# Optimization experiments

Measured on AMD Instinct MI355X. Metric: run time of the kernel, lower is better.

The kernel has to match this reference:

```python
import jax, jax.numpy as jnp
import numpy as np

# Static network layout: inputs occupy columns [0, I), hidden [I, N-O), outputs [N-O, N)
B = 16384  # batch size
N = 1024   # total neurons
I = 128    # input neurons
O = 64     # output neurons
REFRACTORY = 0.9


def _activate(x, act_ids):
    """Vectorized per-neuron heterogeneous activation.
    act_ids: 0=relu, 1=tanh, 2=sigmoid, 3=identity.
    Replaces the original serial per-neuron getattr dispatch loop."""
    r = jax.nn.relu(x)
    t = jnp.tanh(x)
    s = jax.nn.sigmoid(x)
    return jnp.select([act_ids == 0, act_ids == 1, act_ids == 2], [r, t, s], x)


def setup_inputs() -> dict:
    key = jax.random.key(0)
    k0, k1, k2, k3, k4 = jax.random.split(key, 5)
    return {
        "prev_states": jax.random.normal(k0, (B, N), jnp.float32),
        "input_values": jax.random.normal(k1, (B, I), jnp.float32),
        "weight_matrix": jax.random.normal(k2, (N, N), jnp.float32) * 0.05,
        "biases": jax.random.normal(k3, (N,), jnp.float32) * 0.1,
        "act_ids": jax.random.randint(k4, (N,), 0, 4, dtype=jnp.int32),
    }


def reference(prev_states, input_values, weight_matrix, biases, act_ids):
    # _apply_refractory_factor on hidden cols + _assign_input_values on input cols
    states = jnp.concatenate(
        [input_values,
         prev_states[:, I:N - O] * REFRACTORY,
         prev_states[:, N - O:]],
        axis=1)  # [B, N]
    # total_input = states @ W + b
    total = states @ weight_matrix + biases  # [B, N]
    # activation applied to every non-input neuron; input neurons keep their state
    activated = _activate(total, act_ids[None, :])  # [B, N]
    new_states = jnp.concatenate([states[:, :I], activated[:, I:]], axis=1)
    # return output-layer slice
    return new_states[:, N - O:]
```

## Files before the change

### kernel.cpp

```cpp
#include <hip/hip_runtime.h>
#include <math.h>

#define BATCH 16384
#define NN    1024
#define NI    128
#define NO    64
#define REFR  0.9f

typedef float  f32x4  __attribute__((ext_vector_type(4)));
typedef __bf16 bf16x8 __attribute__((ext_vector_type(8)));

__global__ __launch_bounds__(256) void pack_w_kernel(const float* __restrict__ W,
                                                     __bf16* __restrict__ wsB) {
    int idx = blockIdx.x * 256 + threadIdx.x;
    int k = idx >> 6;
    int n = idx & 63;
    float v = W[(size_t)k * NN + (NN - NO) + n];
    int kc = k >> 5;
    if (kc >= 4 && kc < 30) v *= REFR;
    int kk = k & 31;
    int r3 = kk >> 3;
    int j  = kk & 7;
    int tn = n >> 4;
    int l  = r3 * 16 + (n & 15);
    wsB[(size_t)(((kc * 4 + tn) * 64 + l) * 8 + j)] = (__bf16)v;
}

__device__ inline float activate(float x, int id) {
    if (id == 0) return fmaxf(x, 0.0f);
    if (id == 1) return tanhf(x);
    if (id == 2) return 1.0f / (1.0f + __expf(-x));
    return x;
}

__global__ __launch_bounds__(256, 4) void fused_rnn_kernel(
    const float* __restrict__ prev,
    const float* __restrict__ inp,
    const __bf16* __restrict__ wsB,
    const float* __restrict__ bias,
    const int*  __restrict__ act,
    float* __restrict__ out)
{
    const int lane = threadIdx.x & 63;
    const int wv   = threadIdx.x >> 6;
    const int m    = lane & 15;
    const int q    = lane >> 4;
    const int row0 = blockIdx.x * 16;
    const int rowA = row0 + m;

    const float* prow = prev + (size_t)rowA * NN;
    const float* irow = inp  + (size_t)rowA * NI;
    const bf16x8* Bf  = (const bf16x8*)wsB;

    f32x4 acc[4];
    acc[0] = (f32x4){0.f, 0.f, 0.f, 0.f};
    acc[1] = acc[0]; acc[2] = acc[0]; acc[3] = acc[0];

    const int qo = q * 8;

#pragma unroll
    for (int i = 0; i < 8; ++i) {
        const int kc = wv * 8 + i;
        const float* srcRow = (kc < 4) ? irow : prow;

        const float4* p = (const float4*)(srcRow + kc * 32 + qo);
        float4 f0 = p[0];
        float4 f1 = p[1];
        bf16x8 a;
        a[0] = (__bf16)f0.x; a[1] = (__bf16)f0.y;
        a[2] = (__bf16)f0.z; a[3] = (__bf16)f0.w;
        a[4] = (__bf16)f1.x; a[5] = (__bf16)f1.y;
        a[6] = (__bf16)f1.z; a[7] = (__bf16)f1.w;

        const bf16x8* bp = Bf + (size_t)kc * 256 + lane;
        acc[0] = __builtin_amdgcn_mfma_f32_16x16x32_bf16(a, bp[0],   acc[0], 0, 0, 0);
        acc[1] = __builtin_amdgcn_mfma_f32_16x16x32_bf16(a, bp[64],  acc[1], 0, 0, 0);
        acc[2] = __builtin_amdgcn_mfma_f32_16x16x32_bf16(a, bp[128], acc[2], 0, 0, 0);
        acc[3] = __builtin_amdgcn_mfma_f32_16x16x32_bf16(a, bp[192], acc[3], 0, 0, 0);
    }

    __shared__ float red[4][16][68];
#pragma unroll
    for (int t = 0; t < 4; ++t) {
#pragma unroll
        for (int r = 0; r < 4; ++r) {
            red[wv][q * 4 + r][t * 16 + m] = acc[t][r];
        }
    }
    __syncthreads();

    const int orow = threadIdx.x >> 4;
    const int oc   = (threadIdx.x & 15) * 4;

    f32x4 s;
    {
        const f32x4* p0 = (const f32x4*)&red[0][orow][oc];
        const f32x4* p1 = (const f32x4*)&red[1][orow][oc];
        const f32x4* p2 = (const f32x4*)&red[2][orow][oc];
        const f32x4* p3 = (const f32x4*)&red[3][orow][oc];
        s = *p0 + *p1 + *p2 + *p3;
    }

    const float* bo = bias + (NN - NO);
    const int*   ao = act  + (NN - NO);
    f32x4 o;
#pragma unroll
    for (int c = 0; c < 4; ++c) {
        o[c] = activate(s[c] + bo[oc + c], ao[oc + c]);
    }
    *(f32x4*)(out + (size_t)(row0 + orow) * NO + oc) = o;
}

extern "C" void kernel_launch(void* const* d_in, const int* in_sizes, int n_in,
                              void* d_out, int out_size, void* d_ws, size_t ws_size,
                              hipStream_t stream) {
    const float* prev = (const float*)d_in[0];
    const float* inp  = (const float*)d_in[1];
    const float* W    = (const float*)d_in[2];
    const float* bias = (const float*)d_in[3];
    const int*   act  = (const int*)  d_in[4];
    float* out = (float*)d_out;
    __bf16* wsB = (__bf16*)d_ws;

    pack_w_kernel<<<256, 256, 0, stream>>>(W, wsB);

    fused_rnn_kernel<<<BATCH / 16, 256, 0, stream>>>(prev, inp, wsB, bias, act, out);
}
```

Baseline: 114.3 us.

## Process 32 rows per block so each loaded weight fragment feeds two MFMAs

Each block now handles 32 batch rows instead of 16. Every wave computes two 16-row tiles, so each loaded B fragment is reused across two MFMAs, which halves weight-fragment load traffic per row. The grid shrinks to 512 blocks, launch bounds drop to 2 blocks per CU, and the shared reduction buffer doubles. The cost is more registers and fewer blocks, which can weaken latency hiding in a kernel that is mostly bound by the float32 activation reads.

```diff
diff --git a/kernel.cpp b/kernel.cpp
--- a/kernel.cpp
+++ b/kernel.cpp
@@ -33,7 +33,7 @@
     return x;
 }
 
-__global__ __launch_bounds__(256, 4) void fused_rnn_kernel(
+__global__ __launch_bounds__(256, 2) void fused_rnn_kernel(
     const float* __restrict__ prev,
     const float* __restrict__ inp,
     const __bf16* __restrict__ wsB,
@@ -45,70 +45,89 @@
     const int wv   = threadIdx.x >> 6;
     const int m    = lane & 15;
     const int q    = lane >> 4;
-    const int row0 = blockIdx.x * 16;
-    const int rowA = row0 + m;
+    const int row0 = blockIdx.x * 32;
+    const int rowA0 = row0 + m;
+    const int rowA1 = row0 + 16 + m;
 
-    const float* prow = prev + (size_t)rowA * NN;
-    const float* irow = inp  + (size_t)rowA * NI;
-    const bf16x8* Bf  = (const bf16x8*)wsB;
+    const float* prow0 = prev + (size_t)rowA0 * NN;
+    const float* irow0 = inp  + (size_t)rowA0 * NI;
+    const float* prow1 = prev + (size_t)rowA1 * NN;
+    const float* irow1 = inp  + (size_t)rowA1 * NI;
+    const bf16x8* Bf   = (const bf16x8*)wsB;
 
-    f32x4 acc[4];
-    acc[0] = (f32x4){0.f, 0.f, 0.f, 0.f};
-    acc[1] = acc[0]; acc[2] = acc[0]; acc[3] = acc[0];
+    f32x4 acc[2][4];
+#pragma unroll
+    for (int u = 0; u < 2; ++u)
+#pragma unroll
+        for (int t = 0; t < 4; ++t)
+            acc[u][t] = (f32x4){0.f, 0.f, 0.f, 0.f};
 
     const int qo = q * 8;
 
 #pragma unroll
     for (int i = 0; i < 8; ++i) {
         const int kc = wv * 8 + i;
-        const float* srcRow = (kc < 4) ? irow : prow;
+        const float* s0 = (kc < 4) ? irow0 : prow0;
+        const float* s1 = (kc < 4) ? irow1 : prow1;
 
-        const float4* p = (const float4*)(srcRow + kc * 32 + qo);
-        float4 f0 = p[0];
-        float4 f1 = p[1];
-        bf16x8 a;
-        a[0] = (__bf16)f0.x; a[1] = (__bf16)f0.y;
-        a[2] = (__bf16)f0.z; a[3] = (__bf16)f0.w;
-        a[4] = (__bf16)f1.x; a[5] = (__bf16)f1.y;
-        a[6] = (__bf16)f1.z; a[7] = (__bf16)f1.w;
+        const float4* p0 = (const float4*)(s0 + kc * 32 + qo);
+        const float4* p1 = (const float4*)(s1 + kc * 32 + qo);
+        float4 f00 = p0[0], f01 = p0[1];
+        float4 f10 = p1[0], f11 = p1[1];
+
+        bf16x8 a0, a1;
+        a0[0] = (__bf16)f00.x; a0[1] = (__bf16)f00.y;
+        a0[2] = (__bf16)f00.z; a0[3] = (__bf16)f00.w;
+        a0[4] = (__bf16)f01.x; a0[5] = (__bf16)f01.y;
+        a0[6] = (__bf16)f01.z; a0[7] = (__bf16)f01.w;
+        a1[0] = (__bf16)f10.x; a1[1] = (__bf16)f10.y;
+        a1[2] = (__bf16)f10.z; a1[3] = (__bf16)f10.w;
+        a1[4] = (__bf16)f11.x; a1[5] = (__bf16)f11.y;
+        a1[6] = (__bf16)f11.z; a1[7] = (__bf16)f11.w;
 
         const bf16x8* bp = Bf + (size_t)kc * 256 + lane;
-        acc[0] = __builtin_amdgcn_mfma_f32_16x16x32_bf16(a, bp[0],   acc[0], 0, 0, 0);
-        acc[1] = __builtin_amdgcn_mfma_f32_16x16x32_bf16(a, bp[64],  acc[1], 0, 0, 0);
-        acc[2] = __builtin_amdgcn_mfma_f32_16x16x32_bf16(a, bp[128], acc[2], 0, 0, 0);
-        acc[3] = __builtin_amdgcn_mfma_f32_16x16x32_bf16(a, bp[192], acc[3], 0, 0, 0);
+        bf16x8 b0 = bp[0], b1 = bp[64], b2 = bp[128], b3 = bp[192];
+
+        acc[0][0] = __builtin_amdgcn_mfma_f32_16x16x32_bf16(a0, b0, acc[0][0], 0, 0, 0);
+        acc[1][0] = __builtin_amdgcn_mfma_f32_16x16x32_bf16(a1, b0, acc[1][0], 0, 0, 0);
+        acc[0][1] = __builtin_amdgcn_mfma_f32_16x16x32_bf16(a0, b1, acc[0][1], 0, 0, 0);
+        acc[1][1] = __builtin_amdgcn_mfma_f32_16x16x32_bf16(a1, b1, acc[1][1], 0, 0, 0);
+        acc[0][2] = __builtin_amdgcn_mfma_f32_16x16x32_bf16(a0, b2, acc[0][2], 0, 0, 0);
+        acc[1][2] = __builtin_amdgcn_mfma_f32_16x16x32_bf16(a1, b2, acc[1][2], 0, 0, 0);
+        acc[0][3] = __builtin_amdgcn_mfma_f32_16x16x32_bf16(a0, b3, acc[0][3], 0, 0, 0);
+        acc[1][3] = __builtin_amdgcn_mfma_f32_16x16x32_bf16(a1, b3, acc[1][3], 0, 0, 0);
     }
 
-    __shared__ float red[4][16][68];
+    __shared__ float red[4][32][68];
 #pragma unroll
     for (int t = 0; t < 4; ++t) {
 #pragma unroll
         for (int r = 0; r < 4; ++r) {
-            red[wv][q * 4 + r][t * 16 + m] = acc[t][r];
+            red[wv][q * 4 + r][t * 16 + m]      = acc[0][t][r];
+            red[wv][16 + q * 4 + r][t * 16 + m] = acc[1][t][r];
         }
     }
     __syncthreads();
 
     const int orow = threadIdx.x >> 4;
     const int oc   = (threadIdx.x & 15) * 4;
-
-    f32x4 s;
-    {
-        const f32x4* p0 = (const f32x4*)&red[0][orow][oc];
-        const f32x4* p1 = (const f32x4*)&red[1][orow][oc];
-        const f32x4* p2 = (const f32x4*)&red[2][orow][oc];
-        const f32x4* p3 = (const f32x4*)&red[3][orow][oc];
-        s = *p0 + *p1 + *p2 + *p3;
-    }
-
     const float* bo = bias + (NN - NO);
     const int*   ao = act  + (NN - NO);
-    f32x4 o;
+
 #pragma unroll
-    for (int c = 0; c < 4; ++c) {
-        o[c] = activate(s[c] + bo[oc + c], ao[oc + c]);
+    for (int h = 0; h < 2; ++h) {
+        const int rr = orow + h * 16;
+        f32x4 s = *(const f32x4*)&red[0][rr][oc]
+                + *(const f32x4*)&red[1][rr][oc]
+                + *(const f32x4*)&red[2][rr][oc]
+                + *(const f32x4*)&red[3][rr][oc];
+        f32x4 o;
+#pragma unroll
+        for (int c = 0; c < 4; ++c) {
+            o[c] = activate(s[c] + bo[oc + c], ao[oc + c]);
+        }
+        *(f32x4*)(out + (size_t)(row0 + rr) * NO + oc) = o;
     }
-    *(f32x4*)(out + (size_t)(row0 + orow) * NO + oc) = o;
 }
 
 extern "C" void kernel_launch(void* const* d_in, const int* in_sizes, int n_in,
@@ -124,5 +143,5 @@
 
     pack_w_kernel<<<256, 256, 0, stream>>>(W, wsB);
 
-    fused_rnn_kernel<<<BATCH / 16, 256, 0, stream>>>(prev, inp, wsB, bias, act, out);
+    fused_rnn_kernel<<<BATCH / 32, 256, 0, stream>>>(prev, inp, wsB, bias, act, out);
 }
```

Result: no change. 115.2 us (+0.8%).
